# Optimization experiments

Hardware: AMD Instinct MI355X
Metric: run time of the kernel (lower is better)

Reference implementation:

```python
import jax, jax.numpy as jnp
import numpy as np

B, T, C = 2, 4096, 1024
NH, HS, BD, DELTA = 16, 64, 16, 32  # n_head, head_size, bond_dim, horizon window


def setup_inputs() -> dict:
    key = jax.random.key(0)
    ks = jax.random.split(key, 10)
    s = lambda k, shape: jax.random.normal(k, shape, jnp.float32) * 0.02
    return {
        "x": jax.random.normal(ks[0], (B, T, C), jnp.float32),
        "W_disp": s(ks[1], (C, NH * BD)),          # W_disp (no bias)
        "W_val": s(ks[2], (C, C)),                  # W_val (no bias)
        "rel_pos_emb": s(ks[3], (DELTA, BD)),       # rel pos embedding table
        "W_pos": s(ks[4], (BD, BD)),                # pos_proj (no bias)
        "W_sf": s(ks[5], (BD, 2 * BD)),             # strain_fused weight
        "b_sf": jnp.zeros((2 * BD,), jnp.float32),  # strain_fused bias
        "w_bond": s(ks[6], (BD,)),                  # bond_out (no bias)
        "w_dmg": s(ks[7], (BD,)),                   # damage_out weight
        "b_dmg": jnp.full((), -3.0, jnp.float32),   # damage_out bias init -3.0
        "W_cproj": s(ks[8], (C, C)),                # c_proj (no bias)
    }


def reference(x, W_disp, W_val, rel_pos_emb, W_pos, W_sf, b_sf, w_bond, w_dmg, b_dmg, W_cproj):
    Bb, Tt, Cc = x.shape
    delta = DELTA
    gelu = lambda v: jax.nn.gelu(v, approximate=False)

    # projections -> (B, nh, T, *)
    disp = (x @ W_disp).reshape(Bb, Tt, NH, BD).transpose(0, 2, 1, 3)
    val = (x @ W_val).reshape(Bb, Tt, NH, HS).transpose(0, 2, 1, 3)

    idx = jnp.arange(Tt)[:, None] + jnp.arange(delta)[None, :]  # (T, delta) into padded axis
    dpad = jnp.pad(disp, ((0, 0), (0, 0), (delta - 1, 0), (0, 0)))
    win = dpad[:, :, idx, :]                      # (B, nh, T, delta, bd)
    strain = win - disp[:, :, :, None, :]

    pos_feat = rel_pos_emb @ W_pos                # (delta, bd)
    fused = strain @ W_sf + b_sf                  # (B, nh, T, delta, 2bd)
    bf, df = fused[..., :BD], fused[..., BD:]
    bond_logits = gelu(bf + pos_feat) @ w_bond    # (B, nh, T, delta)
    damage = jax.nn.sigmoid(gelu(df) @ w_dmg + b_dmg)
    scores = bond_logits - damage * 10.0

    # causal/left-edge mask: kv_pos = t - delta + 1 + j >= 0
    cmask = (jnp.arange(Tt)[:, None] - delta + 1 + jnp.arange(delta)[None, :]) >= 0
    scores = jnp.where(cmask, scores, -jnp.inf)
    weights = jax.nn.softmax(scores, axis=-1)     # (B, nh, T, delta)

    vpad = jnp.pad(val, ((0, 0), (0, 0), (delta - 1, 0), (0, 0)))
    vw = vpad[:, :, idx, :]                       # (B, nh, T, delta, hs)
    out = jnp.einsum('bntj,bntjh->bnth', weights, vw)
    out = out.transpose(0, 2, 1, 3).reshape(Bb, Tt, Cc)
    return out @ W_cproj                          # resid dropout is eval no-op
```

## Files before the change

kernel.cpp:

```cpp
#include <hip/hip_runtime.h>
#include <hip/hip_bf16.h>

#define BB 2
#define TT 4096
#define CC 1024
#define NH 16
#define HS 64
#define BD 16
#define DELTA 32

typedef unsigned short u16;
typedef unsigned int u32;
typedef __bf16 bf16x8 __attribute__((ext_vector_type(8)));
typedef float floatx4 __attribute__((ext_vector_type(4)));

__device__ __forceinline__ float bf2f(u16 u) {
    unsigned v = ((unsigned)u) << 16;
    return __builtin_bit_cast(float, v);
}
__device__ __forceinline__ u16 f2bf(float x) {
    unsigned u = __builtin_bit_cast(unsigned, x);
    unsigned r = u + 0x7fffu + ((u >> 16) & 1u);
    return (u16)(r >> 16);
}
__device__ __forceinline__ float rcpf(float x) {
    float r;
    asm("v_rcp_f32 %0, %1" : "=v"(r) : "v"(x));
    return r;
}

__device__ __forceinline__ void storeC(float* p, float v) { *p = v; }
__device__ __forceinline__ void storeC(u16* p, float v) { *p = f2bf(v); }

#define GC0 0.3989422804014327f
#define GC1 (-0.06649038006690546f)
#define GC2 0.009973557010035818f
__device__ __forceinline__ float gelup(float x) {
    float u = x * x;
    float p = fmaf(u, fmaf(u, GC2, GC1), GC0);
    return x * fmaf(x, p, 0.5f);
}

__device__ __forceinline__ void load16_lds(const u16* g, u16* l) {
    __builtin_amdgcn_global_load_lds(
        (const __attribute__((address_space(1))) void*)g,
        (__attribute__((address_space(3))) void*)l, 16, 0, 0);
}

#define PREP_CONV   2048
#define PREP_WCAT   (PREP_CONV + 512)
#define PREP_POSF   (PREP_WCAT + 1)
#define PREP_T1     (PREP_POSF + 1024)
#define PREP_TOTAL  (PREP_T1 + 1024)

__global__ __launch_bounds__(256) void fused_prep(
    const float* __restrict__ x,     u16* __restrict__ xbf,
    const float* __restrict__ Wdisp, const float* __restrict__ Wsf,
    const float* __restrict__ rel,   const float* __restrict__ Wpos,
    u16* __restrict__ WcatT,         float* __restrict__ posf,
    const float* __restrict__ Wval,  const float* __restrict__ Wcproj,
    u16* __restrict__ WcpT)
{
    __shared__ u16 tile[32][33];
    const int bi  = blockIdx.x;
    const int tid = threadIdx.x;

    if (bi < PREP_CONV) {
        const long n4 = (long)BB * TT * CC / 4;
        long base = (long)bi * 256 + tid;
        #pragma unroll
        for (int i = 0; i < 4; ++i) {
            long idx = base + (long)i * (PREP_CONV * 256);
            if (idx < n4) {
                float4 v = ((const float4*)x)[idx];
                ushort4 o;
                o.x = f2bf(v.x); o.y = f2bf(v.y); o.z = f2bf(v.z); o.w = f2bf(v.w);
                ((ushort4*)xbf)[idx] = o;
            }
        }
    } else if (bi < PREP_WCAT) {
        const int r = bi - PREP_CONV;
        const int n = r >> 5, o = r & 31;
        float wcol[16];
        #pragma unroll
        for (int d = 0; d < 16; ++d) wcol[d] = Wsf[d * 32 + o];
        for (int c = tid; c < CC; c += 256) {
            float acc = 0.f;
            #pragma unroll
            for (int d = 0; d < 16; ++d)
                acc += Wdisp[c * (NH * BD) + n * 16 + d] * wcol[d];
            WcatT[(long)r * CC + c] = f2bf(acc);
        }
    } else if (bi < PREP_POSF) {
        for (int e = tid; e < DELTA * BD; e += 256) {
            int j = e >> 4, o2 = e & 15;
            float acc = 0.f;
            #pragma unroll
            for (int d = 0; d < 16; ++d)
                acc += rel[j * 16 + d] * Wpos[d * 16 + o2];
            posf[e] = acc;
        }
    } else {
        const bool isV = (bi < PREP_T1);
        const int t = bi - (isV ? PREP_POSF : PREP_T1);
        const float* in = isV ? Wval : Wcproj;
        u16* out = isV ? (WcatT + (size_t)512 * CC) : WcpT;
        const int bx = t & 31, by = t >> 5;
        const int tx = tid & 31, ty = tid >> 5;
        const int xcol = bx * 32 + tx;
        #pragma unroll
        for (int i = 0; i < 4; ++i) {
            int y = by * 32 + ty + i * 8;
            tile[ty + i * 8][tx] = f2bf(in[(long)y * CC + xcol]);
        }
        __syncthreads();
        const int x2 = by * 32 + tx;
        #pragma unroll
        for (int i = 0; i < 4; ++i) {
            int y2 = bx * 32 + ty + i * 8;
            out[(long)y2 * CC + x2] = tile[tx][ty + i * 8];
        }
    }
}

template <typename OUT_T>
__global__ __launch_bounds__(256) void gemm_bt(
    const u16* __restrict__ A, const u16* __restrict__ Bt,
    OUT_T* __restrict__ C, int M, int N, int K)
{
    __shared__ __align__(16) u16 sA[128 * 64];
    __shared__ __align__(16) u16 sB[128 * 64];

    const int tid  = threadIdx.x;
    const int lane = tid & 63;
    const int wave = tid >> 6;
    const int wr = wave >> 1, wc = wave & 1;

    const u32 lin   = blockIdx.y * gridDim.x + blockIdx.x;
    const u32 total = gridDim.x * gridDim.y;
    const u32 qch   = total >> 3;
    const u32 nl    = (lin & 7) * qch + (lin >> 3);
    const int bx    = nl % gridDim.x;
    const int by    = nl / gridDim.x;
    const int m0 = by * 128;
    const int n0 = bx * 128;

    const int sg = tid & 7;
    const int sr = tid >> 3;

    floatx4 acc[4][4] = {};

    for (int k0 = 0; k0 < K; k0 += 64) {
        __syncthreads();
        #pragma unroll
        for (int rnd = 0; rnd < 4; ++rnd) {
            const int r = sr + rnd * 32;
            const int gsw = sg ^ (r & 7);
            load16_lds(A  + (long)(m0 + r) * K + k0 + gsw * 8,
                       &sA[rnd * 2048 + wave * 512]);
            load16_lds(Bt + (long)(n0 + r) * K + k0 + gsw * 8,
                       &sB[rnd * 2048 + wave * 512]);
        }
        __syncthreads();

        #pragma unroll
        for (int kh = 0; kh < 2; ++kh) {
            bf16x8 aF[4], bF[4];
            #pragma unroll
            for (int mt = 0; mt < 4; ++mt) {
                const int rr = wr * 64 + mt * 16 + (lane & 15);
                const int g = (kh * 4 + (lane >> 4)) ^ (rr & 7);
                aF[mt] = *(const bf16x8*)&sA[rr * 64 + g * 8];
            }
            #pragma unroll
            for (int nt = 0; nt < 4; ++nt) {
                const int rr = wc * 64 + nt * 16 + (lane & 15);
                const int g = (kh * 4 + (lane >> 4)) ^ (rr & 7);
                bF[nt] = *(const bf16x8*)&sB[rr * 64 + g * 8];
            }
            #pragma unroll
            for (int mt = 0; mt < 4; ++mt)
                #pragma unroll
                for (int nt = 0; nt < 4; ++nt)
                    acc[mt][nt] = __builtin_amdgcn_mfma_f32_16x16x32_bf16(
                        aF[mt], bF[nt], acc[mt][nt], 0, 0, 0);
        }
    }

    const int rbase = (lane >> 4) << 2;
    const int ccol  = lane & 15;
    #pragma unroll
    for (int mt = 0; mt < 4; ++mt)
        #pragma unroll
        for (int nt = 0; nt < 4; ++nt)
            #pragma unroll
            for (int r = 0; r < 4; ++r) {
                int m  = m0 + wr * 64 + mt * 16 + rbase + r;
                int nn = n0 + wc * 64 + nt * 16 + ccol;
                storeC(C + (long)m * N + nn, acc[mt][nt][r]);
            }
}

__global__ __launch_bounds__(512) void attn_kernel(
    const u16* __restrict__ xcat,
    const float* __restrict__ posf,
    const float* __restrict__ b_sf, const float* __restrict__ w_bond,
    const float* __restrict__ w_dmg, const float* __restrict__ b_dmg,
    u16* __restrict__ att)
{
    __shared__ __align__(16) float sGs[63][36];
    __shared__ __align__(16) float sBias[32][36];
    __shared__ __align__(16) u16 sVT[64 * 64];
    __shared__ __align__(16) u16 sWb[32 * 64];
    __shared__ __align__(16) float sWBv[16], sWDv[16];

    const int tid = threadIdx.x;
    const int t_local = tid >> 5;
    const int j = tid & 31;
    const int t0 = blockIdx.x * 32;
    const int n = blockIdx.y;
    const int b = blockIdx.z;
    const long bT = (long)b * TT;

    const u32* xc = (const u32*)xcat;

    for (int e = tid; e < 63 * 16; e += 512) {
        int r = e >> 4, c = e & 15;
        int tok = t0 - 31 + r;
        u32 w = (tok >= 0) ? xc[(bT + tok) * 768 + n * 16 + c] : 0u;
        float2 f2 = make_float2(bf2f((u16)(w & 0xffffu)), bf2f((u16)(w >> 16)));
        *(float2*)&sGs[r][2 * c] = f2;
    }
    u32* sVT32 = (u32*)sVT;
    for (int e = tid; e < 32 * 32; e += 512) {
        int c = e & 31, rp = e >> 5;
        int tok0 = t0 - 31 + 2 * rp, tok1 = tok0 + 1;
        u32 a  = (tok0 >= 0 && tok0 < TT) ? xc[(bT + tok0) * 768 + 256 + n * 32 + c] : 0u;
        u32 bb = (tok1 >= 0 && tok1 < TT) ? xc[(bT + tok1) * 768 + 256 + n * 32 + c] : 0u;
        u32 lo = (a & 0xffffu) | (bb << 16);
        u32 hi = (a >> 16) | (bb & 0xffff0000u);
        int h0 = 2 * c, h1 = 2 * c + 1;
        int wd0 = (rp & 3) | ((((rp >> 2) ^ h0) & 7) << 2);
        int wd1 = (rp & 3) | ((((rp >> 2) ^ h1) & 7) << 2);
        sVT32[h0 * 32 + wd0] = lo;
        sVT32[h1 * 32 + wd1] = hi;
    }
    u32* sWb32 = (u32*)sWb;
    for (int e = tid; e < 32 * 32; e += 512) sWb32[e] = 0u;
    for (int e = tid; e < 1024; e += 512) {
        int jj = e >> 5, o = e & 31;
        sBias[jj][o] = b_sf[o] + ((o < 16) ? posf[jj * 16 + o] : 0.f);
    }
    if (tid < 16)      sWBv[tid]      = w_bond[tid];
    else if (tid < 32) sWDv[tid - 16] = w_dmg[tid - 16];
    __syncthreads();

    const float bdmg = b_dmg[0];
    float4 bb4[8];
    #pragma unroll
    for (int q = 0; q < 8; ++q) bb4[q] = *(const float4*)&sBias[j][4 * q];

    #pragma unroll
    for (int th = 0; th < 2; ++th) {
        const int tl = t_local + 16 * th;
        const float* Sp = sGs[tl + j];
        const float* Tp = sGs[tl + 31];
        const bool valid = (t0 + tl + j) >= 31;

        float bond = 0.f, dmg = 0.f;
        #pragma unroll
        for (int q = 0; q < 4; ++q) {
            float4 s = *(const float4*)&Sp[4 * q];
            float4 t = *(const float4*)&Tp[4 * q];
            float4 w = *(const float4*)&sWBv[4 * q];
            float4 bbv = bb4[q];
            bond += gelup(s.x - t.x + bbv.x) * w.x;
            bond += gelup(s.y - t.y + bbv.y) * w.y;
            bond += gelup(s.z - t.z + bbv.z) * w.z;
            bond += gelup(s.w - t.w + bbv.w) * w.w;
        }
        #pragma unroll
        for (int q = 0; q < 4; ++q) {
            float4 s = *(const float4*)&Sp[16 + 4 * q];
            float4 t = *(const float4*)&Tp[16 + 4 * q];
            float4 w = *(const float4*)&sWDv[4 * q];
            float4 bbv = bb4[4 + q];
            dmg += gelup(s.x - t.x + bbv.x) * w.x;
            dmg += gelup(s.y - t.y + bbv.y) * w.y;
            dmg += gelup(s.z - t.z + bbv.z) * w.z;
            dmg += gelup(s.w - t.w + bbv.w) * w.w;
        }
        float damage = rcpf(1.f + __expf(-(dmg + bdmg)));
        float score = bond - 10.f * damage;
        float p = valid ? __expf(score) : 0.f;
        float sum = p;
        #pragma unroll
        for (int off = 16; off; off >>= 1) sum += __shfl_xor(sum, off, 32);
        const int k = tl + j;
        const int kk = ((((k >> 3) ^ tl) & 7) << 3) | (k & 7);
        sWb[tl * 64 + kk] = f2bf(p * rcpf(sum));
    }
    __syncthreads();

    const int wave = tid >> 6;
    const int lane = tid & 63;
    const int ttile = wave & 1;
    const int htile = wave >> 1;
    const int fr = lane & 15;
    const int q4 = lane >> 4;
    const int h = htile * 16 + fr;
    const int r = ttile * 16 + fr;

    floatx4 o4 = {0.f, 0.f, 0.f, 0.f};
    #pragma unroll
    for (int ks = 0; ks < 2; ++ks) {
        const int ga = (ks * 4 + q4) ^ (r & 7);
        bf16x8 aF = *(const bf16x8*)&sWb[r * 64 + ga * 8];
        const int gb = (ks * 4 + q4) ^ (h & 7);
        bf16x8 bF = *(const bf16x8*)&sVT[h * 64 + gb * 8];
        o4 = __builtin_amdgcn_mfma_f32_16x16x32_bf16(aF, bF, o4, 0, 0, 0);
    }
    const int trow = ttile * 16 + (q4 << 2);
    const int col = n * 64 + htile * 16 + fr;
    #pragma unroll
    for (int rr = 0; rr < 4; ++rr)
        att[(bT + t0 + trow + rr) * 1024 + col] = f2bf(o4[rr]);
}

extern "C" void kernel_launch(void* const* d_in, const int* in_sizes, int n_in,
                              void* d_out, int out_size, void* d_ws, size_t ws_size,
                              hipStream_t stream)
{
    const float* x      = (const float*)d_in[0];
    const float* Wdisp  = (const float*)d_in[1];
    const float* Wval   = (const float*)d_in[2];
    const float* rel    = (const float*)d_in[3];
    const float* Wpos   = (const float*)d_in[4];
    const float* Wsf    = (const float*)d_in[5];
    const float* bsf    = (const float*)d_in[6];
    const float* wbond  = (const float*)d_in[7];
    const float* wdmg   = (const float*)d_in[8];
    const float* bdmg   = (const float*)d_in[9];
    const float* Wcproj = (const float*)d_in[10];

    char* ws = (char*)d_ws;
    const size_t O_WCAT = 0;
    const size_t O_WCPT = (size_t)4 << 20;
    const size_t O_POSF = (size_t)6 << 20;
    const size_t O_XBF  = (size_t)8 << 20;
    const size_t O_XCAT = (size_t)24 << 20;
    const size_t O_ATT  = (size_t)48 << 20;

    u16*   WcatT = (u16*)(ws + O_WCAT);
    u16*   WcpT  = (u16*)(ws + O_WCPT);
    float* posf  = (float*)(ws + O_POSF);
    u16*   xbf   = (u16*)(ws + O_XBF);
    u16*   xcat  = (u16*)(ws + O_XCAT);
    u16*   att   = (u16*)(ws + O_ATT);

    const int M = BB * TT;

    fused_prep<<<PREP_TOTAL, 256, 0, stream>>>(
        x, xbf, Wdisp, Wsf, rel, Wpos, WcatT, posf, Wval, Wcproj, WcpT);

    gemm_bt<u16><<<dim3(1536 / 128, M / 128), 256, 0, stream>>>(xbf, WcatT, xcat, M, 1536, CC);
    attn_kernel<<<dim3(TT / 32, NH, BB), 512, 0, stream>>>(xcat, posf, bsf, wbond, wdmg, bdmg, att);
    gemm_bt<float><<<dim3(1024 / 128, M / 128), 256, 0, stream>>>(att, WcpT, (float*)d_out, M, 1024, CC);
}
```

Baseline: 208.4 us.

## Double-buffer LDS tiles in bf16 GEMM to overlap global loads with MFMA

```diff
diff --git a/kernel.cpp b/kernel.cpp
--- a/kernel.cpp
+++ b/kernel.cpp
@@ -123,13 +123,48 @@
     }
 }
 
+#define GSTAGE_(BUF, KOFF) do { \
+    _Pragma("unroll") \
+    for (int rnd_ = 0; rnd_ < 4; ++rnd_) { \
+        const int r_ = sr + rnd_ * 32; \
+        const int gsw_ = sg ^ (r_ & 7); \
+        load16_lds(A  + (long)(m0 + r_) * K + (KOFF) + gsw_ * 8, \
+                   &sA[BUF][rnd_ * 2048 + wave * 512]); \
+        load16_lds(Bt + (long)(n0 + r_) * K + (KOFF) + gsw_ * 8, \
+                   &sB[BUF][rnd_ * 2048 + wave * 512]); \
+    } } while (0)
+
+#define GCOMP_(BUF) do { \
+    _Pragma("unroll") \
+    for (int kh_ = 0; kh_ < 2; ++kh_) { \
+        bf16x8 aF_[4], bF_[4]; \
+        _Pragma("unroll") \
+        for (int mt_ = 0; mt_ < 4; ++mt_) { \
+            const int rr_ = wr * 64 + mt_ * 16 + (lane & 15); \
+            const int g_ = (kh_ * 4 + (lane >> 4)) ^ (rr_ & 7); \
+            aF_[mt_] = *(const bf16x8*)&sA[BUF][rr_ * 64 + g_ * 8]; \
+        } \
+        _Pragma("unroll") \
+        for (int nt_ = 0; nt_ < 4; ++nt_) { \
+            const int rr_ = wc * 64 + nt_ * 16 + (lane & 15); \
+            const int g_ = (kh_ * 4 + (lane >> 4)) ^ (rr_ & 7); \
+            bF_[nt_] = *(const bf16x8*)&sB[BUF][rr_ * 64 + g_ * 8]; \
+        } \
+        _Pragma("unroll") \
+        for (int mt_ = 0; mt_ < 4; ++mt_) \
+            _Pragma("unroll") \
+            for (int nt_ = 0; nt_ < 4; ++nt_) \
+                acc[mt_][nt_] = __builtin_amdgcn_mfma_f32_16x16x32_bf16( \
+                    aF_[mt_], bF_[nt_], acc[mt_][nt_], 0, 0, 0); \
+    } } while (0)
+
 template <typename OUT_T>
 __global__ __launch_bounds__(256) void gemm_bt(
     const u16* __restrict__ A, const u16* __restrict__ Bt,
     OUT_T* __restrict__ C, int M, int N, int K)
 {
-    __shared__ __align__(16) u16 sA[128 * 64];
-    __shared__ __align__(16) u16 sB[128 * 64];
+    __shared__ __align__(16) u16 sA[2][128 * 64];
+    __shared__ __align__(16) u16 sB[2][128 * 64];
 
     const int tid  = threadIdx.x;
     const int lane = tid & 63;
@@ -150,41 +185,16 @@
 
     floatx4 acc[4][4] = {};
 
-    for (int k0 = 0; k0 < K; k0 += 64) {
+    GSTAGE_(0, 0);
+    __syncthreads();
+
+    for (int k0 = 0; k0 < K; k0 += 128) {
+        GSTAGE_(1, k0 + 64);
+        GCOMP_(0);
         __syncthreads();
-        #pragma unroll
-        for (int rnd = 0; rnd < 4; ++rnd) {
-            const int r = sr + rnd * 32;
-            const int gsw = sg ^ (r & 7);
-            load16_lds(A  + (long)(m0 + r) * K + k0 + gsw * 8,
-                       &sA[rnd * 2048 + wave * 512]);
-            load16_lds(Bt + (long)(n0 + r) * K + k0 + gsw * 8,
-                       &sB[rnd * 2048 + wave * 512]);
-        }
+        if (k0 + 128 < K) GSTAGE_(0, k0 + 128);
+        GCOMP_(1);
         __syncthreads();
-
-        #pragma unroll
-        for (int kh = 0; kh < 2; ++kh) {
-            bf16x8 aF[4], bF[4];
-            #pragma unroll
-            for (int mt = 0; mt < 4; ++mt) {
-                const int rr = wr * 64 + mt * 16 + (lane & 15);
-                const int g = (kh * 4 + (lane >> 4)) ^ (rr & 7);
-                aF[mt] = *(const bf16x8*)&sA[rr * 64 + g * 8];
-            }
-            #pragma unroll
-            for (int nt = 0; nt < 4; ++nt) {
-                const int rr = wc * 64 + nt * 16 + (lane & 15);
-                const int g = (kh * 4 + (lane >> 4)) ^ (rr & 7);
-                bF[nt] = *(const bf16x8*)&sB[rr * 64 + g * 8];
-            }
-            #pragma unroll
-            for (int mt = 0; mt < 4; ++mt)
-                #pragma unroll
-                for (int nt = 0; nt < 4; ++nt)
-                    acc[mt][nt] = __builtin_amdgcn_mfma_f32_16x16x32_bf16(
-                        aF[mt], bF[nt], acc[mt][nt], 0, 0, 0);
-        }
     }
 
     const int rbase = (lane >> 4) << 2;
@@ -200,6 +210,9 @@
                 storeC(C + (long)m * N + nn, acc[mt][nt][r]);
             }
 }
+
+#undef GSTAGE_
+#undef GCOMP_
 
 __global__ __launch_bounds__(512) void attn_kernel(
     const u16* __restrict__ xcat,
```

After: 224.4 us. 7.7% more time.
